# Performance work log

Hardware: AMD Instinct MI355X
Metric: run time of the kernel (lower is better)

## Reference

```python
import jax, jax.numpy as jnp
import numpy as np

N_NODES = 100000
N_EDGES = 1600000
IN_F, HID, OUT_F = 128, 128, 64
BN_EPS = 1e-5


def _sage_conv(x, src, dst, W_l, b_l, W_r, n_nodes):
    # PyG SAGEConv (aggr='mean', root_weight=True):
    #   out_i = W_l @ mean_{j in N(i)} x_j + b_l + W_r @ x_i
    msg = x[src]                                             # [E, d] gather
    agg = jax.ops.segment_sum(msg, dst, num_segments=n_nodes)  # [N, d]
    deg = jax.ops.segment_sum(jnp.ones((src.shape[0],), x.dtype), dst,
                              num_segments=n_nodes)          # [N]
    agg = agg / jnp.clip(deg, 1.0)[:, None]
    return agg @ W_l.T + b_l + x @ W_r.T


def setup_inputs() -> dict:
    key = jax.random.key(0)
    ks = jax.random.split(key, 10)
    x = jax.random.normal(ks[0], (N_NODES, IN_F), dtype=jnp.float32)
    edge_index = jax.random.randint(ks[1], (2, N_EDGES), 0, N_NODES, dtype=jnp.int64)
    s = 0.05
    return {
        "x": x,
        "edge_index": edge_index,
        "W1_l": jax.random.normal(ks[2], (HID, IN_F), dtype=jnp.float32) * s,
        "b1": jnp.zeros((HID,), jnp.float32),
        "W1_r": jax.random.normal(ks[3], (HID, IN_F), dtype=jnp.float32) * s,
        "bn_gamma": jnp.ones((HID,), jnp.float32),
        "bn_beta": jnp.zeros((HID,), jnp.float32),
        "bn_mean": jax.random.normal(ks[4], (HID,), dtype=jnp.float32) * 0.1,
        "bn_var": jnp.ones((HID,), jnp.float32),
        "W2_l": jax.random.normal(ks[5], (OUT_F, HID), dtype=jnp.float32) * s,
        "b2": jnp.zeros((OUT_F,), jnp.float32),
        "W2_r": jax.random.normal(ks[6], (OUT_F, HID), dtype=jnp.float32) * s,
    }


def reference(x, edge_index, W1_l, b1, W1_r, bn_gamma, bn_beta, bn_mean, bn_var,
              W2_l, b2, W2_r):
    src, dst = edge_index[0], edge_index[1]
    n = x.shape[0]
    # eval mode: dropout = identity
    h = _sage_conv(x, src, dst, W1_l, b1, W1_r, n)            # [N, HID]
    # BatchNorm1d (eval, running stats)
    h = (h - bn_mean) * jax.lax.rsqrt(bn_var + BN_EPS) * bn_gamma + bn_beta
    h = jax.nn.relu(h)
    return _sage_conv(h, src, dst, W2_l, b2, W2_r, n)         # [N, OUT_F]
```

## Files before the change

### kernel.cpp

```cpp
#include <hip/hip_runtime.h>

#define FEAT 128
#define BN_EPS 1e-5f
#define P_CNT 1024
#define BKT_SHIFT 9
#define BKT_NODES 512

typedef __attribute__((ext_vector_type(8))) short s8frag;
typedef __attribute__((ext_vector_type(4))) float f4frag;

union FragU { uint4 u; s8frag v; };

__device__ __forceinline__ unsigned short f2bf(float f) {
    unsigned u = __float_as_uint(f);
    unsigned r = (u + 0x7fffu + ((u >> 16) & 1u)) >> 16;
    return (unsigned short)r;
}
__device__ __forceinline__ void unpack2(unsigned d, float& lo, float& hi) {
    lo = __uint_as_float(d << 16);
    hi = __uint_as_float(d & 0xffff0000u);
}
__device__ __forceinline__ void acc8(float* acc, uint4 d) {
    float l, h;
    unpack2(d.x, l, h); acc[0] += l; acc[1] += h;
    unpack2(d.y, l, h); acc[2] += l; acc[3] += h;
    unpack2(d.z, l, h); acc[4] += l; acc[5] += h;
    unpack2(d.w, l, h); acc[6] += l; acc[7] += h;
}

__global__ __launch_bounds__(256) void front2(
    const int* __restrict__ dst, int E, int per, int NB,
    unsigned* __restrict__ histT,
    const float* __restrict__ x, unsigned short* __restrict__ xb, int XB,
    const float* __restrict__ W1l, const float* __restrict__ W1r,
    const float* __restrict__ W2l, const float* __restrict__ W2r,
    const float* __restrict__ b1, const float* __restrict__ g,
    const float* __restrict__ bt, const float* __restrict__ mu,
    const float* __restrict__ var, const float* __restrict__ b2,
    unsigned short* __restrict__ Wb1, unsigned short* __restrict__ Wb2,
    float* __restrict__ bnsc, float* __restrict__ bnsh, float* __restrict__ cb2)
{
    const int bid = blockIdx.x;
    const int tid = threadIdx.x;
    if (bid < P_CNT) {
        __shared__ unsigned h[256];
        for (int i = tid; i < NB; i += 256) h[i] = 0u;
        __syncthreads();
        int s = bid * per;
        int e1 = min(E, s + per);
        for (int e = s + tid; e < e1; e += 256)
            atomicAdd(&h[((unsigned)dst[e]) >> BKT_SHIFT], 1u);
        __syncthreads();
        for (int i = tid; i < NB; i += 256)
            histT[(size_t)i * P_CNT + bid] = h[i];
    } else if (bid < P_CNT + XB) {
        int t = (bid - P_CNT) * 256 + tid;
        const float4* src = (const float4*)(x) + (size_t)t * 2;
        float4 a = src[0], b = src[1];
        uint4 o;
        o.x = f2bf(a.x) | ((unsigned)f2bf(a.y) << 16);
        o.y = f2bf(a.z) | ((unsigned)f2bf(a.w) << 16);
        o.z = f2bf(b.x) | ((unsigned)f2bf(b.y) << 16);
        o.w = f2bf(b.z) | ((unsigned)f2bf(b.w) << 16);
        ((uint4*)xb)[t] = o;
    } else {
        int idx = (bid - P_CNT - XB) * 256 + tid;
        if (idx < 128 * 256) {
            int n = idx >> 8, k = idx & 255;
            float w = (k < 128) ? W1l[n * 128 + k] : W1r[n * 128 + (k - 128)];
            Wb1[idx] = f2bf(w);
        }
        if (idx < 128 * 128) {
            int n = idx >> 7, k = idx & 127;
            float w = (n < 64) ? W2l[n * 128 + k] : W2r[(n - 64) * 128 + k];
            Wb2[idx] = f2bf(w);
        }
        if (idx < 128) {
            float sc = rsqrtf(var[idx] + BN_EPS) * g[idx];
            bnsc[idx] = sc;
            bnsh[idx] = sc * (b1[idx] - mu[idx]) + bt[idx];
            cb2[idx] = (idx < 64) ? 0.f : b2[idx - 64];
        }
    }
}

__global__ void scan_block_c(const unsigned* __restrict__ in, unsigned* __restrict__ excl,
                             unsigned* __restrict__ partials, int M) {
    __shared__ unsigned buf[256];
    int i = blockIdx.x * 256 + threadIdx.x;
    unsigned v = (i < M) ? in[i] : 0u;
    buf[threadIdx.x] = v;
    __syncthreads();
    for (int off = 1; off < 256; off <<= 1) {
        unsigned t = (threadIdx.x >= (unsigned)off) ? buf[threadIdx.x - off] : 0u;
        __syncthreads();
        buf[threadIdx.x] += t;
        __syncthreads();
    }
    if (i < M) excl[i] = buf[threadIdx.x] - v;
    if (threadIdx.x == 255) partials[blockIdx.x] = buf[255];
}

__global__ void scan_finish(unsigned* __restrict__ arr,
                            const unsigned* __restrict__ partials, int M, int E) {
    __shared__ unsigned red[256];
    int b = blockIdx.x;
    unsigned s = 0;
    for (int t = threadIdx.x; t < b; t += 256) s += partials[t];
    red[threadIdx.x] = s;
    __syncthreads();
    for (int off = 128; off > 0; off >>= 1) {
        if ((int)threadIdx.x < off) red[threadIdx.x] += red[threadIdx.x + off];
        __syncthreads();
    }
    unsigned base = red[0];
    int i = b * 256 + threadIdx.x;
    if (i < M) arr[i] += base;
    if (i == 0) arr[M] = (unsigned)E;
}

__global__ __launch_bounds__(256) void scatter_bucket(
    const int* __restrict__ src, const int* __restrict__ dst, int E, int per, int NB,
    const unsigned* __restrict__ hexcl, unsigned* __restrict__ buck)
{
    __shared__ unsigned cnt[256];
    const int p = blockIdx.x, tid = threadIdx.x;
    for (int i = tid; i < NB; i += 256) cnt[i] = hexcl[(size_t)i * P_CNT + p];
    __syncthreads();
    int s = p * per, e1 = min(E, s + per);
    for (int e = s + tid; e < e1; e += 256) {
        unsigned d = (unsigned)dst[e];
        unsigned pos = atomicAdd(&cnt[d >> BKT_SHIFT], 1u);
        buck[pos] = ((unsigned)src[e] << BKT_SHIFT) | (d & (BKT_NODES - 1u));
    }
}

__global__ __launch_bounds__(512) void bucket_csr(
    const unsigned* __restrict__ buck, const unsigned* __restrict__ hexcl,
    unsigned* __restrict__ row_start, unsigned* __restrict__ csr_src, int N, int E)
{
    __shared__ unsigned h[BKT_NODES];
    __shared__ unsigned sc[BKT_NODES];
    const int b = blockIdx.x, tid = threadIdx.x;
    const unsigned bs = hexcl[(size_t)b * P_CNT];
    const unsigned be = hexcl[(size_t)(b + 1) * P_CNT];
    h[tid] = 0u;
    __syncthreads();
    for (unsigned e = bs + tid; e < be; e += BKT_NODES)
        atomicAdd(&h[buck[e] & (BKT_NODES - 1u)], 1u);
    __syncthreads();
    unsigned v = h[tid];
    sc[tid] = v;
    __syncthreads();
    for (int off = 1; off < BKT_NODES; off <<= 1) {
        unsigned t = (tid >= off) ? sc[tid - off] : 0u;
        __syncthreads();
        sc[tid] += t;
        __syncthreads();
    }
    unsigned pos0 = bs + sc[tid] - v;
    int node = b * BKT_NODES + tid;
    if (node < N) row_start[node] = pos0;
    h[tid] = pos0;
    __syncthreads();
    for (unsigned e = bs + tid; e < be; e += BKT_NODES) {
        unsigned pk = buck[e];
        unsigned pos = atomicAdd(&h[pk & (BKT_NODES - 1u)], 1u);
        csr_src[pos] = pk >> BKT_SHIFT;
    }
    if (b == 0 && tid == 0) row_start[N] = (unsigned)E;
}

__global__ __launch_bounds__(256) void gather_mean_bf(const unsigned short* __restrict__ xb,
                                                      const unsigned* __restrict__ row_start,
                                                      const unsigned* __restrict__ csr_src,
                                                      unsigned short* __restrict__ aggb,
                                                      int N, int NBLK) {
    const int bid = blockIdx.x;
    const int half = (bid >> 2) & 1;
    const int nodeblk = (bid & 3) | ((bid >> 3) << 2);
    if (nodeblk >= NBLK) return;
    const int node = nodeblk * 32 + (threadIdx.x >> 3);
    if (node >= N) return;
    const int f = half * 64 + (threadIdx.x & 7) * 8;
    unsigned s0 = row_start[node], s1 = row_start[node + 1];
    float acc[8];
#pragma unroll
    for (int i = 0; i < 8; i++) acc[i] = 0.f;
    unsigned i = s0;
    for (; i + 8 <= s1; i += 8) {
        unsigned i0 = csr_src[i + 0], i1 = csr_src[i + 1];
        unsigned i2 = csr_src[i + 2], i3 = csr_src[i + 3];
        unsigned i4 = csr_src[i + 4], i5 = csr_src[i + 5];
        unsigned i6 = csr_src[i + 6], i7 = csr_src[i + 7];
        uint4 d0 = *(const uint4*)(xb + (size_t)i0 * 128 + f);
        uint4 d1 = *(const uint4*)(xb + (size_t)i1 * 128 + f);
        uint4 d2 = *(const uint4*)(xb + (size_t)i2 * 128 + f);
        uint4 d3 = *(const uint4*)(xb + (size_t)i3 * 128 + f);
        uint4 d4 = *(const uint4*)(xb + (size_t)i4 * 128 + f);
        uint4 d5 = *(const uint4*)(xb + (size_t)i5 * 128 + f);
        uint4 d6 = *(const uint4*)(xb + (size_t)i6 * 128 + f);
        uint4 d7 = *(const uint4*)(xb + (size_t)i7 * 128 + f);
        acc8(acc, d0); acc8(acc, d1); acc8(acc, d2); acc8(acc, d3);
        acc8(acc, d4); acc8(acc, d5); acc8(acc, d6); acc8(acc, d7);
    }
    if (i + 4 <= s1) {
        unsigned i0 = csr_src[i + 0], i1 = csr_src[i + 1];
        unsigned i2 = csr_src[i + 2], i3 = csr_src[i + 3];
        uint4 d0 = *(const uint4*)(xb + (size_t)i0 * 128 + f);
        uint4 d1 = *(const uint4*)(xb + (size_t)i1 * 128 + f);
        uint4 d2 = *(const uint4*)(xb + (size_t)i2 * 128 + f);
        uint4 d3 = *(const uint4*)(xb + (size_t)i3 * 128 + f);
        acc8(acc, d0); acc8(acc, d1); acc8(acc, d2); acc8(acc, d3);
        i += 4;
    }
    if (i + 2 <= s1) {
        unsigned i0 = csr_src[i + 0], i1 = csr_src[i + 1];
        uint4 d0 = *(const uint4*)(xb + (size_t)i0 * 128 + f);
        uint4 d1 = *(const uint4*)(xb + (size_t)i1 * 128 + f);
        acc8(acc, d0); acc8(acc, d1);
        i += 2;
    }
    if (i < s1) {
        unsigned i0 = csr_src[i];
        uint4 d0 = *(const uint4*)(xb + (size_t)i0 * 128 + f);
        acc8(acc, d0);
    }
    float inv = (s1 > s0) ? 1.0f / (float)(s1 - s0) : 0.f;
    uint4 o;
    o.x = f2bf(acc[0] * inv) | ((unsigned)f2bf(acc[1] * inv) << 16);
    o.y = f2bf(acc[2] * inv) | ((unsigned)f2bf(acc[3] * inv) << 16);
    o.z = f2bf(acc[4] * inv) | ((unsigned)f2bf(acc[5] * inv) << 16);
    o.w = f2bf(acc[6] * inv) | ((unsigned)f2bf(acc[7] * inv) << 16);
    *(uint4*)(aggb + (size_t)node * 128 + f) = o;
}

__global__ __launch_bounds__(256) void sage_dense(
    const unsigned short* __restrict__ aggb,
    const unsigned short* __restrict__ xb,
    const unsigned short* __restrict__ Wb1,
    const unsigned short* __restrict__ Wb2,
    const float* __restrict__ bnsc, const float* __restrict__ bnsh,
    const float* __restrict__ cb2,
    unsigned short* __restrict__ uvb, int N)
{
    __shared__ __align__(16) unsigned short As[64 * 128];
    uint4* AsV = (uint4*)As;

    const int tid = threadIdx.x;
    const int wave = tid >> 6;
    const int lane = tid & 63;
    const int mr = lane & 15;
    const int q = lane >> 4;
    const int m0 = blockIdx.x * 64;
    const int mw = m0 + wave * 16 + mr;
    const bool mv = mw < N;

    FragU ag[4], ax[4];
#pragma unroll
    for (int kc4 = 0; kc4 < 4; kc4++) {
        ag[kc4].u = make_uint4(0u, 0u, 0u, 0u);
        ax[kc4].u = make_uint4(0u, 0u, 0u, 0u);
        if (mv) {
            ag[kc4].u = *(const uint4*)(aggb + (size_t)mw * 128 + kc4 * 32 + q * 8);
            ax[kc4].u = *(const uint4*)(xb + (size_t)mw * 128 + kc4 * 32 + q * 8);
        }
    }

    f4frag acc[8];
#pragma unroll
    for (int j = 0; j < 8; j++)
#pragma unroll
        for (int r = 0; r < 4; r++) acc[j][r] = 0.f;

#pragma unroll
    for (int kc4 = 0; kc4 < 4; kc4++) {
#pragma unroll
        for (int j = 0; j < 8; j++) {
            FragU b;
            b.u = *(const uint4*)(Wb1 + (size_t)(j * 16 + mr) * 256 + kc4 * 32 + q * 8);
            acc[j] = __builtin_amdgcn_mfma_f32_16x16x32_bf16(ag[kc4].v, b.v, acc[j], 0, 0, 0);
        }
    }
#pragma unroll
    for (int kc4 = 0; kc4 < 4; kc4++) {
#pragma unroll
        for (int j = 0; j < 8; j++) {
            FragU b;
            b.u = *(const uint4*)(Wb1 + (size_t)(j * 16 + mr) * 256 + 128 + kc4 * 32 + q * 8);
            acc[j] = __builtin_amdgcn_mfma_f32_16x16x32_bf16(ax[kc4].v, b.v, acc[j], 0, 0, 0);
        }
    }

#pragma unroll
    for (int j = 0; j < 8; j++) {
        int n = j * 16 + mr;
        float sc = bnsc[n], sh = bnsh[n];
        int cn = n >> 3;
#pragma unroll
        for (int r = 0; r < 4; r++) {
            int ml = wave * 16 + q * 4 + r;
            float v = fmaxf(acc[j][r] * sc + sh, 0.f);
            As[(ml * 16 + (cn ^ (ml & 15))) * 8 + (n & 7)] = f2bf(v);
        }
    }
    __syncthreads();

#pragma unroll
    for (int j = 0; j < 8; j++)
#pragma unroll
        for (int r = 0; r < 4; r++) acc[j][r] = 0.f;
    const int arow = (wave * 16 + mr) * 16;
#pragma unroll
    for (int kc4 = 0; kc4 < 4; kc4++) {
        FragU a;
        a.u = AsV[arow + ((kc4 * 4 + q) ^ mr)];
#pragma unroll
        for (int j = 0; j < 8; j++) {
            FragU b;
            b.u = *(const uint4*)(Wb2 + (size_t)(j * 16 + mr) * 128 + kc4 * 32 + q * 8);
            acc[j] = __builtin_amdgcn_mfma_f32_16x16x32_bf16(a.v, b.v, acc[j], 0, 0, 0);
        }
    }

#pragma unroll
    for (int j = 0; j < 8; j++) {
        int n = j * 16 + mr;
        float cb = cb2[n];
#pragma unroll
        for (int r = 0; r < 4; r++) {
            int mrow = m0 + wave * 16 + q * 4 + r;
            if (mrow < N)
                uvb[(size_t)mrow * 128 + n] = f2bf(acc[j][r] + cb);
        }
    }
}

__global__ __launch_bounds__(256) void gather_out_bf(const unsigned short* __restrict__ uvb,
                                                     const unsigned* __restrict__ row_start,
                                                     const unsigned* __restrict__ csr_src,
                                                     float* __restrict__ out, int N) {
    int gid = blockIdx.x * 256 + threadIdx.x;
    int node = gid >> 3;
    if (node >= N) return;
    int f = (threadIdx.x & 7) * 8;
    unsigned s0 = row_start[node], s1 = row_start[node + 1];
    float acc[8];
#pragma unroll
    for (int i = 0; i < 8; i++) acc[i] = 0.f;
    unsigned i = s0;
    for (; i + 8 <= s1; i += 8) {
        unsigned i0 = csr_src[i + 0], i1 = csr_src[i + 1];
        unsigned i2 = csr_src[i + 2], i3 = csr_src[i + 3];
        unsigned i4 = csr_src[i + 4], i5 = csr_src[i + 5];
        unsigned i6 = csr_src[i + 6], i7 = csr_src[i + 7];
        uint4 d0 = *(const uint4*)(uvb + (size_t)i0 * 128 + f);
        uint4 d1 = *(const uint4*)(uvb + (size_t)i1 * 128 + f);
        uint4 d2 = *(const uint4*)(uvb + (size_t)i2 * 128 + f);
        uint4 d3 = *(const uint4*)(uvb + (size_t)i3 * 128 + f);
        uint4 d4 = *(const uint4*)(uvb + (size_t)i4 * 128 + f);
        uint4 d5 = *(const uint4*)(uvb + (size_t)i5 * 128 + f);
        uint4 d6 = *(const uint4*)(uvb + (size_t)i6 * 128 + f);
        uint4 d7 = *(const uint4*)(uvb + (size_t)i7 * 128 + f);
        acc8(acc, d0); acc8(acc, d1); acc8(acc, d2); acc8(acc, d3);
        acc8(acc, d4); acc8(acc, d5); acc8(acc, d6); acc8(acc, d7);
    }
    if (i + 4 <= s1) {
        unsigned i0 = csr_src[i + 0], i1 = csr_src[i + 1];
        unsigned i2 = csr_src[i + 2], i3 = csr_src[i + 3];
        uint4 d0 = *(const uint4*)(uvb + (size_t)i0 * 128 + f);
        uint4 d1 = *(const uint4*)(uvb + (size_t)i1 * 128 + f);
        uint4 d2 = *(const uint4*)(uvb + (size_t)i2 * 128 + f);
        uint4 d3 = *(const uint4*)(uvb + (size_t)i3 * 128 + f);
        acc8(acc, d0); acc8(acc, d1); acc8(acc, d2); acc8(acc, d3);
        i += 4;
    }
    if (i + 2 <= s1) {
        unsigned i0 = csr_src[i + 0], i1 = csr_src[i + 1];
        uint4 d0 = *(const uint4*)(uvb + (size_t)i0 * 128 + f);
        uint4 d1 = *(const uint4*)(uvb + (size_t)i1 * 128 + f);
        acc8(acc, d0); acc8(acc, d1);
        i += 2;
    }
    if (i < s1) {
        unsigned i0 = csr_src[i];
        uint4 d0 = *(const uint4*)(uvb + (size_t)i0 * 128 + f);
        acc8(acc, d0);
    }
    float inv = (s1 > s0) ? 1.0f / (float)(s1 - s0) : 0.f;
    uint4 dv = *(const uint4*)(uvb + (size_t)node * 128 + 64 + f);
    float vv[8];
    unpack2(dv.x, vv[0], vv[1]);
    unpack2(dv.y, vv[2], vv[3]);
    unpack2(dv.z, vv[4], vv[5]);
    unpack2(dv.w, vv[6], vv[7]);
    float4 o0 = make_float4(acc[0] * inv + vv[0], acc[1] * inv + vv[1],
                            acc[2] * inv + vv[2], acc[3] * inv + vv[3]);
    float4 o1 = make_float4(acc[4] * inv + vv[4], acc[5] * inv + vv[5],
                            acc[6] * inv + vv[6], acc[7] * inv + vv[7]);
    *(float4*)(out + (size_t)node * 64 + f) = o0;
    *(float4*)(out + (size_t)node * 64 + f + 4) = o1;
}

extern "C" void kernel_launch(void* const* d_in, const int* in_sizes, int n_in,
                              void* d_out, int out_size, void* d_ws, size_t ws_size,
                              hipStream_t stream) {
    const float* x     = (const float*)d_in[0];
    const int*   edge  = (const int*)d_in[1];
    const float* W1l   = (const float*)d_in[2];
    const float* b1    = (const float*)d_in[3];
    const float* W1r   = (const float*)d_in[4];
    const float* gamma = (const float*)d_in[5];
    const float* beta  = (const float*)d_in[6];
    const float* mean  = (const float*)d_in[7];
    const float* var   = (const float*)d_in[8];
    const float* W2l   = (const float*)d_in[9];
    const float* b2    = (const float*)d_in[10];
    const float* W2r   = (const float*)d_in[11];

    const int N = in_sizes[0] / FEAT;
    const int E = in_sizes[1] / 2;
    const int* srcI = edge;
    const int* dstI = edge + E;

    const int NB  = (N + BKT_NODES - 1) >> BKT_SHIFT;
    const int M   = NB * P_CNT;
    const int per = (E + P_CNT - 1) / P_CNT;

    unsigned short* uvb  = (unsigned short*)d_ws;
    unsigned short* aggb = uvb + (size_t)N * 128;
    unsigned short* xb   = aggb + (size_t)N * 128;
    unsigned short* Wb1  = xb + (size_t)N * 128;
    unsigned short* Wb2  = Wb1 + 256 * 128;
    float* bnsc = (float*)(Wb2 + 128 * 128);
    float* bnsh = bnsc + 128;
    float* cb2  = bnsh + 128;
    unsigned* histT     = (unsigned*)(cb2 + 128);
    unsigned* hexcl     = histT + (M + 1);
    unsigned* partials  = hexcl + (M + 1);
    unsigned* row_start = partials + 1024;
    unsigned* buck      = row_start + (N + 1);
    unsigned* csr_src   = buck + E;

    float* outp = (float*)d_out;

    const int total8 = N * FEAT / 8;
    const int XB = (total8 + 255) / 256;
    const int PB = (128 * 256 + 255) / 256;
    front2<<<P_CNT + XB + PB, 256, 0, stream>>>(
        dstI, E, per, NB, histT, x, xb, XB,
        W1l, W1r, W2l, W2r, b1, gamma, beta, mean, var, b2,
        Wb1, Wb2, bnsc, bnsh, cb2);

    scan_block_c<<<M / 256, 256, 0, stream>>>(histT, hexcl, partials, M);
    scan_finish<<<M / 256, 256, 0, stream>>>(hexcl, partials, M, E);
    scatter_bucket<<<P_CNT, 256, 0, stream>>>(srcI, dstI, E, per, NB, hexcl, buck);
    bucket_csr<<<NB, BKT_NODES, 0, stream>>>(buck, hexcl, row_start, csr_src, N, E);

    {
        const int NBLK = (N + 31) / 32;
        const int G = 8 * ((2 * NBLK + 7) / 8);
        gather_mean_bf<<<G, 256, 0, stream>>>(xb, row_start, csr_src, aggb, N, NBLK);
    }
    sage_dense<<<(N + 63) / 64, 256, 0, stream>>>(aggb, xb, Wb1, Wb2, bnsc, bnsh, cb2, uvb, N);
    gather_out_bf<<<(N * 8 + 255) / 256, 256, 0, stream>>>(uvb, row_start, csr_src, outp, N);
}
```

Measured before the change: 340.3 us.

## Stage weights in LDS and make sage_dense a persistent grid-stride kernel

sage_dense now copies both layer weight matrices into swizzled shared memory once per block and loops over 128-row tiles with a persistent grid capped at 256 blocks of 512 threads. B fragments come from LDS instead of repeated global or L2 loads. The aim is to cut redundant weight traffic and per-block launch overhead. It uses 128 KB of LDS, which limits occupancy to one block per CU, and adds an extra barrier per tile.

```diff
diff --git a/kernel.cpp b/kernel.cpp
--- a/kernel.cpp
+++ b/kernel.cpp
@@ -235,7 +235,7 @@
     *(uint4*)(aggb + (size_t)node * 128 + f) = o;
 }
 
-__global__ __launch_bounds__(256) void sage_dense(
+__global__ __launch_bounds__(512) void sage_dense(
     const unsigned short* __restrict__ aggb,
     const unsigned short* __restrict__ xb,
     const unsigned short* __restrict__ Wb1,
@@ -244,95 +244,117 @@
     const float* __restrict__ cb2,
     unsigned short* __restrict__ uvb, int N)
 {
-    __shared__ __align__(16) unsigned short As[64 * 128];
-    uint4* AsV = (uint4*)As;
+    __shared__ __align__(16) unsigned short W1a[128 * 128];
+    __shared__ __align__(16) unsigned short W1b[128 * 128];
+    __shared__ __align__(16) unsigned short W2s[128 * 128];
+    __shared__ __align__(16) unsigned short As[128 * 128];
+    uint4* W1aV = (uint4*)W1a;
+    uint4* W1bV = (uint4*)W1b;
+    uint4* W2sV = (uint4*)W2s;
+    uint4* AsV  = (uint4*)As;
 
     const int tid = threadIdx.x;
     const int wave = tid >> 6;
     const int lane = tid & 63;
     const int mr = lane & 15;
     const int q = lane >> 4;
-    const int m0 = blockIdx.x * 64;
-    const int mw = m0 + wave * 16 + mr;
-    const bool mv = mw < N;
-
-    FragU ag[4], ax[4];
-#pragma unroll
-    for (int kc4 = 0; kc4 < 4; kc4++) {
-        ag[kc4].u = make_uint4(0u, 0u, 0u, 0u);
-        ax[kc4].u = make_uint4(0u, 0u, 0u, 0u);
-        if (mv) {
-            ag[kc4].u = *(const uint4*)(aggb + (size_t)mw * 128 + kc4 * 32 + q * 8);
-            ax[kc4].u = *(const uint4*)(xb + (size_t)mw * 128 + kc4 * 32 + q * 8);
-        }
-    }
-
-    f4frag acc[8];
-#pragma unroll
-    for (int j = 0; j < 8; j++)
-#pragma unroll
-        for (int r = 0; r < 4; r++) acc[j][r] = 0.f;
-
-#pragma unroll
-    for (int kc4 = 0; kc4 < 4; kc4++) {
+
+#pragma unroll
+    for (int i = 0; i < 4; i++) {
+        int gch = tid + i * 512;
+        int n = gch >> 4, c = gch & 15;
+        int slot = n * 16 + (c ^ (n & 15));
+        W1aV[slot] = *(const uint4*)(Wb1 + (size_t)n * 256 + c * 8);
+        W1bV[slot] = *(const uint4*)(Wb1 + (size_t)n * 256 + 128 + c * 8);
+        W2sV[slot] = *(const uint4*)(Wb2 + (size_t)n * 128 + c * 8);
+    }
+    __syncthreads();
+
+    const int nTiles = (N + 127) >> 7;
+    for (int t = blockIdx.x; t < nTiles; t += gridDim.x) {
+        const int m0 = t * 128;
+        const int mw = m0 + wave * 16 + mr;
+        const bool mv = mw < N;
+
+        FragU ag[4], ax[4];
+#pragma unroll
+        for (int kc4 = 0; kc4 < 4; kc4++) {
+            ag[kc4].u = make_uint4(0u, 0u, 0u, 0u);
+            ax[kc4].u = make_uint4(0u, 0u, 0u, 0u);
+            if (mv) {
+                ag[kc4].u = *(const uint4*)(aggb + (size_t)mw * 128 + kc4 * 32 + q * 8);
+                ax[kc4].u = *(const uint4*)(xb + (size_t)mw * 128 + kc4 * 32 + q * 8);
+            }
+        }
+
+        f4frag acc[8];
+#pragma unroll
+        for (int j = 0; j < 8; j++)
+#pragma unroll
+            for (int r = 0; r < 4; r++) acc[j][r] = 0.f;
+
+#pragma unroll
+        for (int kc4 = 0; kc4 < 4; kc4++) {
+#pragma unroll
+            for (int j = 0; j < 8; j++) {
+                FragU b;
+                b.u = W1aV[(j * 16 + mr) * 16 + ((kc4 * 4 + q) ^ mr)];
+                acc[j] = __builtin_amdgcn_mfma_f32_16x16x32_bf16(ag[kc4].v, b.v, acc[j], 0, 0, 0);
+            }
+        }
+#pragma unroll
+        for (int kc4 = 0; kc4 < 4; kc4++) {
+#pragma unroll
+            for (int j = 0; j < 8; j++) {
+                FragU b;
+                b.u = W1bV[(j * 16 + mr) * 16 + ((kc4 * 4 + q) ^ mr)];
+                acc[j] = __builtin_amdgcn_mfma_f32_16x16x32_bf16(ax[kc4].v, b.v, acc[j], 0, 0, 0);
+            }
+        }
+
 #pragma unroll
         for (int j = 0; j < 8; j++) {
-            FragU b;
-            b.u = *(const uint4*)(Wb1 + (size_t)(j * 16 + mr) * 256 + kc4 * 32 + q * 8);
-            acc[j] = __builtin_amdgcn_mfma_f32_16x16x32_bf16(ag[kc4].v, b.v, acc[j], 0, 0, 0);
-        }
-    }
-#pragma unroll
-    for (int kc4 = 0; kc4 < 4; kc4++) {
+            int n = j * 16 + mr;
+            float sc = bnsc[n], sh = bnsh[n];
+            int cn = n >> 3;
+#pragma unroll
+            for (int r = 0; r < 4; r++) {
+                int ml = wave * 16 + q * 4 + r;
+                float v = fmaxf(acc[j][r] * sc + sh, 0.f);
+                As[(ml * 16 + (cn ^ (ml & 15))) * 8 + (n & 7)] = f2bf(v);
+            }
+        }
+        __syncthreads();
+
+#pragma unroll
+        for (int j = 0; j < 8; j++)
+#pragma unroll
+            for (int r = 0; r < 4; r++) acc[j][r] = 0.f;
+        const int arow = (wave * 16 + mr) * 16;
+#pragma unroll
+        for (int kc4 = 0; kc4 < 4; kc4++) {
+            FragU a;
+            a.u = AsV[arow + ((kc4 * 4 + q) ^ mr)];
+#pragma unroll
+            for (int j = 0; j < 8; j++) {
+                FragU b;
+                b.u = W2sV[(j * 16 + mr) * 16 + ((kc4 * 4 + q) ^ mr)];
+                acc[j] = __builtin_amdgcn_mfma_f32_16x16x32_bf16(a.v, b.v, acc[j], 0, 0, 0);
+            }
+        }
+
 #pragma unroll
         for (int j = 0; j < 8; j++) {
-            FragU b;
-            b.u = *(const uint4*)(Wb1 + (size_t)(j * 16 + mr) * 256 + 128 + kc4 * 32 + q * 8);
-            acc[j] = __builtin_amdgcn_mfma_f32_16x16x32_bf16(ax[kc4].v, b.v, acc[j], 0, 0, 0);
-        }
-    }
-
-#pragma unroll
-    for (int j = 0; j < 8; j++) {
-        int n = j * 16 + mr;
-        float sc = bnsc[n], sh = bnsh[n];
-        int cn = n >> 3;
-#pragma unroll
-        for (int r = 0; r < 4; r++) {
-            int ml = wave * 16 + q * 4 + r;
-            float v = fmaxf(acc[j][r] * sc + sh, 0.f);
-            As[(ml * 16 + (cn ^ (ml & 15))) * 8 + (n & 7)] = f2bf(v);
-        }
-    }
-    __syncthreads();
-
-#pragma unroll
-    for (int j = 0; j < 8; j++)
-#pragma unroll
-        for (int r = 0; r < 4; r++) acc[j][r] = 0.f;
-    const int arow = (wave * 16 + mr) * 16;
-#pragma unroll
-    for (int kc4 = 0; kc4 < 4; kc4++) {
-        FragU a;
-        a.u = AsV[arow + ((kc4 * 4 + q) ^ mr)];
-#pragma unroll
-        for (int j = 0; j < 8; j++) {
-            FragU b;
-            b.u = *(const uint4*)(Wb2 + (size_t)(j * 16 + mr) * 128 + kc4 * 32 + q * 8);
-            acc[j] = __builtin_amdgcn_mfma_f32_16x16x32_bf16(a.v, b.v, acc[j], 0, 0, 0);
-        }
-    }
-
-#pragma unroll
-    for (int j = 0; j < 8; j++) {
-        int n = j * 16 + mr;
-        float cb = cb2[n];
-#pragma unroll
-        for (int r = 0; r < 4; r++) {
-            int mrow = m0 + wave * 16 + q * 4 + r;
-            if (mrow < N)
-                uvb[(size_t)mrow * 128 + n] = f2bf(acc[j][r] + cb);
-        }
+            int n = j * 16 + mr;
+            float cb = cb2[n];
+#pragma unroll
+            for (int r = 0; r < 4; r++) {
+                int mrow = m0 + wave * 16 + q * 4 + r;
+                if (mrow < N)
+                    uvb[(size_t)mrow * 128 + n] = f2bf(acc[j][r] + cb);
+            }
+        }
+        __syncthreads();
     }
 }
 
@@ -462,6 +484,10 @@
         const int G = 8 * ((2 * NBLK + 7) / 8);
         gather_mean_bf<<<G, 256, 0, stream>>>(xb, row_start, csr_src, aggb, N, NBLK);
     }
-    sage_dense<<<(N + 63) / 64, 256, 0, stream>>>(aggb, xb, Wb1, Wb2, bnsc, bnsh, cb2, uvb, N);
+    {
+        const int nTiles = (N + 127) / 128;
+        const int G = nTiles < 256 ? nTiles : 256;
+        sage_dense<<<G, 512, 0, stream>>>(aggb, xb, Wb1, Wb2, bnsc, bnsh, cb2, uvb, N);
+    }
     gather_out_bf<<<(N * 8 + 255) / 256, 256, 0, stream>>>(uvb, row_start, csr_src, outp, N);
 }
```

Result: faster. 278.7 us (-18.1%).
